# Optimization experiments

Hardware: AMD Instinct MI355X
Metric: run time of the kernel (lower is better)

Reference implementation:

```python
import jax, jax.numpy as jnp
import numpy as np

B, S, D, H, FF = 4, 2048, 512, 8, 2048
HD = D // H
WINDOW = 64  # local attention half-window in rank space
EPS = 1e-5


def _layer_norm(v, g, b):
    m = jnp.mean(v, axis=-1, keepdims=True)
    var = jnp.mean(jnp.square(v - m), axis=-1, keepdims=True)
    return (v - m) / jnp.sqrt(var + EPS) * g + b


def setup_inputs() -> dict:
    key = jax.random.key(0)
    ks = jax.random.split(key, 10)
    sc = 0.02
    x = jax.random.normal(ks[0], (B, S, D), jnp.float32)
    padding_mask = jnp.zeros((B, S), dtype=bool)
    i = jnp.arange(S)
    local = jnp.abs(i[:, None] - i[None, :]) <= WINDOW
    glob = (i[:, None] == 0) | (i[None, :] == 0)  # global spectrum token at pos 0
    attn_mask = jnp.where(local | glob, 0.0, -jnp.inf).astype(jnp.float32)
    return {
        "x": x,
        "padding_mask": padding_mask,
        "attn_mask": attn_mask,
        "in_proj_w": jax.random.normal(ks[1], (3 * D, D), jnp.float32) * sc,
        "in_proj_b": jnp.zeros((3 * D,), jnp.float32),
        "out_proj_w": jax.random.normal(ks[2], (D, D), jnp.float32) * sc,
        "out_proj_b": jnp.zeros((D,), jnp.float32),
        "ln1_g": jnp.ones((D,), jnp.float32),
        "ln1_b": jnp.zeros((D,), jnp.float32),
        "ln2_g": jnp.ones((D,), jnp.float32),
        "ln2_b": jnp.zeros((D,), jnp.float32),
        "ff_w1": jax.random.normal(ks[3], (FF, D), jnp.float32) * sc,
        "ff_b1": jnp.zeros((FF,), jnp.float32),
        "ff_w2": jax.random.normal(ks[4], (D, FF), jnp.float32) * sc,
        "ff_b2": jnp.zeros((D,), jnp.float32),
    }


def reference(x, padding_mask, attn_mask, in_proj_w, in_proj_b, out_proj_w,
              out_proj_b, ln1_g, ln1_b, ln2_g, ln2_b, ff_w1, ff_b1, ff_w2, ff_b2):
    # pre-LN attention
    a = _layer_norm(x, ln1_g, ln1_b)
    qkv = a @ in_proj_w.T + in_proj_b  # [B,S,3D]
    q, k, v = jnp.split(qkv, 3, axis=-1)
    to_heads = lambda t: t.reshape(B, S, H, HD).transpose(0, 2, 1, 3)
    q, k, v = to_heads(q), to_heads(k), to_heads(v)
    scores = jnp.einsum('bhqd,bhkd->bhqk', q, k) * (HD ** -0.5)
    # float attn_mask path: key_padding_mask converted to additive -inf floats
    kpm = jnp.where(padding_mask, -jnp.inf, 0.0).astype(scores.dtype)
    scores = scores + attn_mask[None, None, :, :] + kpm[:, None, None, :]
    p = jax.nn.softmax(scores, axis=-1)
    o = jnp.einsum('bhqk,bhkd->bhqd', p, v).transpose(0, 2, 1, 3).reshape(B, S, D)
    o = o @ out_proj_w.T + out_proj_b
    x = x + o  # residual (dropout = 0)
    # pre-LN feed-forward with exact GELU (torch nn.GELU default)
    f = _layer_norm(x, ln2_g, ln2_b)
    f = jax.nn.gelu(f @ ff_w1.T + ff_b1, approximate=False) @ ff_w2.T + ff_b2
    return x + f
```

## Files before the change

kernel.cpp:

```cpp
#include <hip/hip_runtime.h>
#include <hip/hip_bf16.h>
#include <math.h>

namespace {

constexpr int kB = 4, kS = 2048, kD = 512, kH = 8, kFF = 2048;
constexpr int kM = kB * kS;
constexpr int kHD = kD / kH;
constexpr int kWin = 64;

typedef __attribute__((ext_vector_type(8))) short short8;
typedef __attribute__((ext_vector_type(4))) float f32x4;

__device__ __forceinline__ float bf2f(__hip_bfloat16 v) { return __bfloat162float(v); }
__device__ __forceinline__ __hip_bfloat16 f2bf(float v) { return __float2bfloat16(v); }
__device__ __forceinline__ int iclamp(int v, int lo, int hi) { return v < lo ? lo : (v > hi ? hi : v); }

__device__ __forceinline__ void async16(const void* g, void* l) {
  __builtin_amdgcn_global_load_lds((const __attribute__((address_space(1))) void*)g,
                                   (__attribute__((address_space(3))) void*)l, 16, 0, 0);
}

__global__ __launch_bounds__(256)
void prep(const float* __restrict__ iw, const float* __restrict__ ow,
          const float* __restrict__ f1, const float* __restrict__ f2,
          __hip_bfloat16* __restrict__ wq, __hip_bfloat16* __restrict__ wo,
          __hip_bfloat16* __restrict__ w1, __hip_bfloat16* __restrict__ w2,
          const float* __restrict__ x, const float* __restrict__ g,
          const float* __restrict__ bta, __hip_bfloat16* __restrict__ a,
          __hip_bfloat16* __restrict__ xb) {
  const int id = blockIdx.x;
  if (id < 3072) {
    const float* s; __hip_bfloat16* d; int base;
    if (id < 768)       { s = iw; d = wq; base = id; }
    else if (id < 1024) { s = ow; d = wo; base = id - 768; }
    else if (id < 2048) { s = f1; d = w1; base = id - 1024; }
    else                { s = f2; d = w2; base = id - 2048; }
    int i = base * 1024 + threadIdx.x * 4;
    float4 v = *(const float4*)(s + i);
    union { __hip_bfloat16 h[4]; uint2 u; } t;
    t.h[0] = f2bf(v.x); t.h[1] = f2bf(v.y); t.h[2] = f2bf(v.z); t.h[3] = f2bf(v.w);
    *(uint2*)(d + i) = t.u;
  } else {
    int row = (id - 3072) * 4 + (threadIdx.x >> 6);
    int lane = threadIdx.x & 63;
    const float* xr = x + (size_t)row * kD;
    int c = lane * 8;
    float4 v0 = *(const float4*)(xr + c);
    float4 v1 = *(const float4*)(xr + c + 4);
    union { __hip_bfloat16 h[8]; int4 u; } xr8;
    xr8.h[0] = f2bf(v0.x); xr8.h[1] = f2bf(v0.y); xr8.h[2] = f2bf(v0.z); xr8.h[3] = f2bf(v0.w);
    xr8.h[4] = f2bf(v1.x); xr8.h[5] = f2bf(v1.y); xr8.h[6] = f2bf(v1.z); xr8.h[7] = f2bf(v1.w);
    *(int4*)(xb + (size_t)row * kD + c) = xr8.u;
    float s  = v0.x + v0.y + v0.z + v0.w + v1.x + v1.y + v1.z + v1.w;
    float ss = v0.x*v0.x + v0.y*v0.y + v0.z*v0.z + v0.w*v0.w
             + v1.x*v1.x + v1.y*v1.y + v1.z*v1.z + v1.w*v1.w;
#pragma unroll
    for (int o = 32; o > 0; o >>= 1) { s += __shfl_xor(s, o); ss += __shfl_xor(ss, o); }
    float mean = s * (1.0f / kD);
    float inv  = rsqrtf(ss * (1.0f / kD) - mean * mean + 1e-5f);
    float4 g0 = *(const float4*)(g + c),   g1 = *(const float4*)(g + c + 4);
    float4 b0 = *(const float4*)(bta + c), b1 = *(const float4*)(bta + c + 4);
    union { __hip_bfloat16 h[8]; int4 u; } t;
    t.h[0] = f2bf((v0.x - mean) * inv * g0.x + b0.x);
    t.h[1] = f2bf((v0.y - mean) * inv * g0.y + b0.y);
    t.h[2] = f2bf((v0.z - mean) * inv * g0.z + b0.z);
    t.h[3] = f2bf((v0.w - mean) * inv * g0.w + b0.w);
    t.h[4] = f2bf((v1.x - mean) * inv * g1.x + b1.x);
    t.h[5] = f2bf((v1.y - mean) * inv * g1.y + b1.y);
    t.h[6] = f2bf((v1.z - mean) * inv * g1.z + b1.z);
    t.h[7] = f2bf((v1.w - mean) * inv * g1.w + b1.w);
    *(int4*)(a + (size_t)row * kD + c) = t.u;
  }
}

__global__ __launch_bounds__(256)
void ln_rows_bf(const __hip_bfloat16* __restrict__ x, const float* __restrict__ g,
                const float* __restrict__ bta, __hip_bfloat16* __restrict__ out) {
  int row = blockIdx.x * 4 + (threadIdx.x >> 6);
  int lane = threadIdx.x & 63;
  int c = lane * 8;
  union { short8 v; __hip_bfloat16 hh[8]; } u;
  u.v = *(const short8*)(x + (size_t)row * kD + c);
  float f[8];
  float s = 0.f, ss = 0.f;
#pragma unroll
  for (int i = 0; i < 8; ++i) { f[i] = bf2f(u.hh[i]); s += f[i]; ss += f[i] * f[i]; }
#pragma unroll
  for (int o = 32; o > 0; o >>= 1) { s += __shfl_xor(s, o); ss += __shfl_xor(ss, o); }
  float mean = s * (1.0f / kD);
  float inv  = rsqrtf(ss * (1.0f / kD) - mean * mean + 1e-5f);
  float4 g0 = *(const float4*)(g + c),   g1 = *(const float4*)(g + c + 4);
  float4 b0 = *(const float4*)(bta + c), b1 = *(const float4*)(bta + c + 4);
  union { __hip_bfloat16 h[8]; int4 v; } t;
  t.h[0] = f2bf((f[0] - mean) * inv * g0.x + b0.x);
  t.h[1] = f2bf((f[1] - mean) * inv * g0.y + b0.y);
  t.h[2] = f2bf((f[2] - mean) * inv * g0.z + b0.z);
  t.h[3] = f2bf((f[3] - mean) * inv * g0.w + b0.w);
  t.h[4] = f2bf((f[4] - mean) * inv * g1.x + b1.x);
  t.h[5] = f2bf((f[5] - mean) * inv * g1.y + b1.y);
  t.h[6] = f2bf((f[6] - mean) * inv * g1.z + b1.z);
  t.h[7] = f2bf((f[7] - mean) * inv * g1.w + b1.w);
  *(int4*)(out + (size_t)row * kD + c) = t.v;
}

__global__ __launch_bounds__(256)
void attn_tile(const __hip_bfloat16* __restrict__ qkv, const __hip_bfloat16* __restrict__ vt,
               __hip_bfloat16* __restrict__ o) {
  const int bh = blockIdx.x;
  const int b = bh >> 3, h = bh & 7;
  const int tid = threadIdx.x;
  const int lane = tid & 63, w = tid >> 6;

  __shared__ alignas(16) char smem[4 * 160 * 20 * 2];

  const __hip_bfloat16* base = qkv + (size_t)b * kS * (3 * kD);
  const __hip_bfloat16* vt_bh = vt + (size_t)(b * kH + h) * kHD * kS;

  if (blockIdx.y == 0) {
    float* sc   = (float*)smem;
    float* qs   = sc + 2048;
    float* redm = qs + 64;
    float* reds = redm + 4;
    float* part = reds + 4;
    if (tid < kHD) qs[tid] = bf2f(base[h * kHD + tid]) * 0.125f;
    __syncthreads();

    float m = -1e30f;
#pragma unroll
    for (int it = 0; it < 8; ++it) {
      int k = it * 256 + tid;
      const short8* kp = (const short8*)(base + (size_t)k * (3 * kD) + kD + h * kHD);
      float s = 0.f;
#pragma unroll
      for (int cc = 0; cc < 8; ++cc) {
        union { short8 v; __hip_bfloat16 hh[8]; } u;
        u.v = kp[cc];
#pragma unroll
        for (int d = 0; d < 8; ++d) s += qs[cc * 8 + d] * bf2f(u.hh[d]);
      }
      sc[k] = s;
      m = fmaxf(m, s);
    }
#pragma unroll
    for (int off = 32; off > 0; off >>= 1) m = fmaxf(m, __shfl_xor(m, off));
    if (lane == 0) redm[w] = m;
    __syncthreads();
    float M = fmaxf(fmaxf(redm[0], redm[1]), fmaxf(redm[2], redm[3]));

    float ls = 0.f;
#pragma unroll
    for (int it = 0; it < 8; ++it) {
      int k = it * 256 + tid;
      float e = __expf(sc[k] - M);
      sc[k] = e;
      ls += e;
    }
#pragma unroll
    for (int off = 32; off > 0; off >>= 1) ls += __shfl_xor(ls, off);
    if (lane == 0) reds[w] = ls;
    __syncthreads();
    float L = reds[0] + reds[1] + reds[2] + reds[3];

    float a0 = 0.f, a1 = 0.f;
    const __hip_bfloat16* vr = vt_bh + (size_t)lane * kS + w * 512;
#pragma unroll
    for (int c = 0; c < 64; c += 2) {
      union { short8 v; __hip_bfloat16 hh[8]; } u0, u1;
      u0.v = *(const short8*)(vr + c * 8);
      u1.v = *(const short8*)(vr + c * 8 + 8);
#pragma unroll
      for (int j = 0; j < 8; ++j) {
        a0 += sc[w * 512 + c * 8 + j] * bf2f(u0.hh[j]);
        a1 += sc[w * 512 + c * 8 + 8 + j] * bf2f(u1.hh[j]);
      }
    }
    part[w * 64 + lane] = a0 + a1;
    __syncthreads();
    if (tid < kHD) {
      float s = part[tid] + part[64 + tid] + part[128 + tid] + part[192 + tid];
      o[(size_t)(b * kS) * kD + h * kHD + tid] = f2bf(s / L);
    }
    return;
  }

  const int tq = (blockIdx.y - 1) * 4 + w;
  const int quad = lane >> 4, col = lane & 15;
  const int q0 = tq * 16;
  const int kbase = q0 - kWin;
  __hip_bfloat16* Pt = (__hip_bfloat16*)smem + w * 160 * 20;

  short8 aq0, aq1;
  {
    const __hip_bfloat16* qrow = base + (size_t)(q0 + col) * (3 * kD) + h * kHD + quad * 8;
    aq0 = *(const short8*)qrow;
    aq1 = *(const short8*)(qrow + 32);
  }

  f32x4 sc[10];
#pragma unroll
  for (int t = 0; t < 10; ++t) {
    int krow = (t < 9) ? iclamp(kbase + t * 16 + col, 0, kS - 1) : col;
    const short8* kp = (const short8*)(base + (size_t)krow * (3 * kD) + kD + h * kHD + quad * 8);
    f32x4 a = (f32x4){0.f, 0.f, 0.f, 0.f};
    a = __builtin_amdgcn_mfma_f32_16x16x32_bf16(aq0, kp[0], a, 0, 0, 0);
    a = __builtin_amdgcn_mfma_f32_16x16x32_bf16(aq1, kp[4], a, 0, 0, 0);
    sc[t] = a;
  }

  float rowmax[4] = {-1e30f, -1e30f, -1e30f, -1e30f};
#pragma unroll
  for (int t = 0; t < 10; ++t) {
#pragma unroll
    for (int r = 0; r < 4; ++r) {
      int q = q0 + quad * 4 + r;
      bool valid;
      if (t < 9) {
        int k = kbase + t * 16 + col;
        valid = (k >= 0) && (k < kS) && ((q - k <= kWin && k - q <= kWin) || k == 0);
      } else {
        valid = (col == 0) && (kbase > 0);
      }
      float s = valid ? sc[t][r] * 0.125f : -1e30f;
      sc[t][r] = s;
      rowmax[r] = fmaxf(rowmax[r], s);
    }
  }
#pragma unroll
  for (int r = 0; r < 4; ++r)
#pragma unroll
    for (int off = 1; off < 16; off <<= 1)
      rowmax[r] = fmaxf(rowmax[r], __shfl_xor(rowmax[r], off));

  float rowsum[4] = {0.f, 0.f, 0.f, 0.f};
#pragma unroll
  for (int t = 0; t < 10; ++t)
#pragma unroll
    for (int r = 0; r < 4; ++r) {
      float e = __expf(sc[t][r] - rowmax[r]);
      sc[t][r] = e;
      rowsum[r] += e;
    }
#pragma unroll
  for (int r = 0; r < 4; ++r)
#pragma unroll
    for (int off = 1; off < 16; off <<= 1)
      rowsum[r] += __shfl_xor(rowsum[r], off);

#pragma unroll
  for (int t = 0; t < 10; ++t) {
    union { ushort u[4]; unsigned long long ll; } pk;
#pragma unroll
    for (int r = 0; r < 4; ++r) {
      __hip_bfloat16 hv = f2bf(sc[t][r]);
      pk.u[r] = *(ushort*)&hv;
    }
    *(unsigned long long*)&Pt[(t * 16 + col) * 20 + quad * 4] = pk.ll;
  }

  f32x4 oacc[4];
#pragma unroll
  for (int n = 0; n < 4; ++n) oacc[n] = (f32x4){0.f, 0.f, 0.f, 0.f};

#pragma unroll
  for (int c = 0; c < 5; ++c) {
    union { short s[8]; short8 v; } pa;
#pragma unroll
    for (int j = 0; j < 8; ++j) pa.s[j] = *(const short*)&Pt[(c * 32 + quad * 8 + j) * 20 + col];
    const int kc = c * 32 + quad * 8;
    const int kstart = (kc < 144) ? iclamp(kbase + kc, 0, kS - 8) : (kc - 144);
#pragma unroll
    for (int n = 0; n < 4; ++n) {
      short8 vb = *(const short8*)(vt_bh + (size_t)(n * 16 + col) * kS + kstart);
      oacc[n] = __builtin_amdgcn_mfma_f32_16x16x32_bf16(pa.v, vb, oacc[n], 0, 0, 0);
    }
  }

#pragma unroll
  for (int n = 0; n < 4; ++n)
#pragma unroll
    for (int r = 0; r < 4; ++r) {
      int q = q0 + quad * 4 + r;
      if (q == 0) continue;
      o[(size_t)(b * kS + q) * kD + h * kHD + n * 16 + col] = f2bf(oacc[n][r] / rowsum[r]);
    }
}

template <int TM, int TN, int NB, int EPI, int WVT, typename OT, typename RT>
__global__ __launch_bounds__(256, 4)
void gemm_bt(const __hip_bfloat16* __restrict__ A, const __hip_bfloat16* __restrict__ W,
             const float* __restrict__ bias, const RT* __restrict__ resid,
             OT* __restrict__ C, __hip_bfloat16* __restrict__ vt, int Ndim, int K) {
  constexpr int MI = TM / 32;
  constexpr int NF = TN / 32;
  __shared__ __hip_bfloat16 As[TM * 64];
  __shared__ __hip_bfloat16 Ws[TN * 64];

  const int id = blockIdx.x;
  const int rr = id & 7, tt = id >> 3;
  const int nb = tt % NB, mb = (tt / NB) * 8 + rr;

  const int tid = threadIdx.x;
  const int lane = tid & 63, w = tid >> 6;
  const int wm = w >> 1, wn = w & 1;
  const int quad = lane >> 4, mrow = lane & 15;
  const int m0 = mb * TM, n0 = nb * TN;

  const int lrow = lane >> 3;
  const int lcol = ((lane & 7) ^ lrow) << 3;

  f32x4 acc[MI][NF];
#pragma unroll
  for (int i = 0; i < MI; ++i)
#pragma unroll
    for (int j = 0; j < NF; ++j) acc[i][j] = (f32x4){0.f, 0.f, 0.f, 0.f};

  for (int kt = 0; kt < K; kt += 64) {
#pragma unroll
    for (int it = 0; it < MI; ++it) {
      int c = w * MI + it;
      async16(A + (size_t)(m0 + c * 8 + lrow) * K + kt + lcol, &As[c * 512]);
    }
#pragma unroll
    for (int it = 0; it < NF; ++it) {
      int c = w * NF + it;
      async16(W + (size_t)(n0 + c * 8 + lrow) * K + kt + lcol, &Ws[c * 512]);
    }
    __syncthreads();
#pragma unroll
    for (int kk = 0; kk < 64; kk += 32) {
      const int ch = (kk >> 3) + quad;
      const int sw = (ch ^ (mrow & 7)) << 3;
      short8 af[MI], wf[NF];
#pragma unroll
      for (int i = 0; i < MI; ++i)
        af[i] = *(const short8*)&As[(wm * (TM / 2) + i * 16 + mrow) * 64 + sw];
#pragma unroll
      for (int j = 0; j < NF; ++j)
        wf[j] = *(const short8*)&Ws[(wn * (TN / 2) + j * 16 + mrow) * 64 + sw];
#pragma unroll
      for (int i = 0; i < MI; ++i)
#pragma unroll
        for (int j = 0; j < NF; ++j)
          acc[i][j] = __builtin_amdgcn_mfma_f32_16x16x32_bf16(af[i], wf[j], acc[i][j], 0, 0, 0);
    }
    __syncthreads();
  }

  if constexpr (WVT) {
    if (n0 >= 1024) {
      __hip_bfloat16* Ls = As;
      const int bb = m0 >> 11, ss0 = m0 & (kS - 1);
      const int n0v = n0 - 1024;
#pragma unroll
      for (int p = 0; p < 2; ++p) {
        __syncthreads();
#pragma unroll
        for (int jj = 0; jj < 2; ++jj) {
          int j = p * 2 + jj;
          int lr = wn * 32 + jj * 16 + mrow;
          float bs = bias[1024 + n0v + wn * 64 + j * 16 + mrow];
#pragma unroll
          for (int i = 0; i < 4; ++i) {
            int tok = wm * 64 + i * 16 + quad * 4;
            int tw = tok ^ ((lr & 15) << 3);
            union { __hip_bfloat16 h[4]; unsigned long long u; } pk;
#pragma unroll
            for (int r = 0; r < 4; ++r) pk.h[r] = f2bf(acc[i][j][r] + bs);
            *(unsigned long long*)&Ls[lr * 128 + tw] = pk.u;
          }
        }
        __syncthreads();
#pragma unroll
        for (int i2 = 0; i2 < 4; ++i2) {
          int c = i2 * 256 + tid;
          int lr = c >> 4, off = (c & 15) << 3;
          int tw = off ^ ((lr & 15) << 3);
          short8 v = *(const short8*)&Ls[lr * 128 + tw];
          int colv = (lr >> 5) * 64 + p * 32 + (lr & 31);
          *(short8*)(vt + (size_t)(bb * 512 + n0v + colv) * kS + ss0 + off) = v;
        }
      }
      return;
    }
  }

#pragma unroll
  for (int i = 0; i < MI; ++i) {
#pragma unroll
    for (int r = 0; r < 4; ++r) {
      int row = m0 + wm * (TM / 2) + i * 16 + quad * 4 + r;
#pragma unroll
      for (int j = 0; j < NF; ++j) {
        int col = n0 + wn * (TN / 2) + j * 16 + mrow;
        float v = acc[i][j][r] + bias[col];
        if (EPI == 1) v = 0.5f * v * (1.0f + erff(v * 0.70710678118f));
        if (EPI == 3) v += bf2f(((const __hip_bfloat16*)resid)[(size_t)row * Ndim + col]);
        if constexpr (__is_same(OT, float)) C[(size_t)row * Ndim + col] = v;
        else                                C[(size_t)row * Ndim + col] = f2bf(v);
      }
    }
  }
}

}

extern "C" void kernel_launch(void* const* d_in, const int* in_sizes, int n_in,
                              void* d_out, int out_size, void* d_ws, size_t ws_size,
                              hipStream_t stream) {
  const float* x          = (const float*)d_in[0];
  const float* in_proj_w  = (const float*)d_in[3];
  const float* in_proj_b  = (const float*)d_in[4];
  const float* out_proj_w = (const float*)d_in[5];
  const float* out_proj_b = (const float*)d_in[6];
  const float* ln1_g      = (const float*)d_in[7];
  const float* ln1_b      = (const float*)d_in[8];
  const float* ln2_g      = (const float*)d_in[9];
  const float* ln2_b      = (const float*)d_in[10];
  const float* ff_w1      = (const float*)d_in[11];
  const float* ff_b1      = (const float*)d_in[12];
  const float* ff_w2      = (const float*)d_in[13];
  const float* ff_b2      = (const float*)d_in[14];
  float* out = (float*)d_out;

  char* ws = (char*)d_ws;
  size_t off = 0;
  auto carve = [&](size_t bytes) { char* p = ws + off; off += (bytes + 255) & ~(size_t)255; return p; };
  __hip_bfloat16* wqkv_bf = (__hip_bfloat16*)carve((size_t)3 * kD * kD * 2);
  __hip_bfloat16* wout_bf = (__hip_bfloat16*)carve((size_t)kD * kD * 2);
  __hip_bfloat16* wff1_bf = (__hip_bfloat16*)carve((size_t)kFF * kD * 2);
  __hip_bfloat16* wff2_bf = (__hip_bfloat16*)carve((size_t)kD * kFF * 2);
  __hip_bfloat16* a_bf    = (__hip_bfloat16*)carve((size_t)kM * kD * 2);
  __hip_bfloat16* x_bf    = (__hip_bfloat16*)carve((size_t)kM * kD * 2);
  __hip_bfloat16* qkv_bf  = (__hip_bfloat16*)carve((size_t)kM * 3 * kD * 2);
  __hip_bfloat16* vt      = (__hip_bfloat16*)carve((size_t)kM * kD * 2);
  __hip_bfloat16* o_bf    = (__hip_bfloat16*)carve((size_t)kM * kD * 2);
  __hip_bfloat16* r1b     = (__hip_bfloat16*)carve((size_t)kM * kD * 2);
  __hip_bfloat16* ln2_bf  = (__hip_bfloat16*)carve((size_t)kM * kD * 2);
  __hip_bfloat16* ff1_bf  = (__hip_bfloat16*)carve((size_t)kM * kFF * 2);

  prep<<<5120, 256, 0, stream>>>(in_proj_w, out_proj_w, ff_w1, ff_w2,
                                 wqkv_bf, wout_bf, wff1_bf, wff2_bf,
                                 x, ln1_g, ln1_b, a_bf, x_bf);
  gemm_bt<128, 128, 12, 0, 1, __hip_bfloat16, float><<<64 * 12, 256, 0, stream>>>(
      a_bf, wqkv_bf, in_proj_b, nullptr, qkv_bf, vt, 3 * kD, kD);
  attn_tile<<<dim3(kB * kH, kS / 64 + 1), 256, 0, stream>>>(qkv_bf, vt, o_bf);
  gemm_bt<64, 64, 8, 3, 0, __hip_bfloat16, __hip_bfloat16><<<128 * 8, 256, 0, stream>>>(
      o_bf, wout_bf, out_proj_b, x_bf, r1b, nullptr, kD, kD);
  ln_rows_bf<<<kM / 4, 256, 0, stream>>>(r1b, ln2_g, ln2_b, ln2_bf);
  gemm_bt<128, 128, 16, 1, 0, __hip_bfloat16, float><<<64 * 16, 256, 0, stream>>>(
      ln2_bf, wff1_bf, ff_b1, nullptr, ff1_bf, nullptr, kFF, kD);
  gemm_bt<64, 64, 8, 3, 0, float, __hip_bfloat16><<<128 * 8, 256, 0, stream>>>(
      ff1_bf, wff2_bf, ff_b2, r1b, out, nullptr, kD, kFF);
}
```

Measured before the change: 239.1 us.

## Stage shared K tile in LDS for local attention and restructure global-row dot

```diff
diff --git a/kernel.cpp b/kernel.cpp
--- a/kernel.cpp
+++ b/kernel.cpp
@@ -112,34 +112,36 @@
   const int tid = threadIdx.x;
   const int lane = tid & 63, w = tid >> 6;
 
-  __shared__ alignas(16) char smem[4 * 160 * 20 * 2];
+  __shared__ alignas(16) char smem[26880];
 
   const __hip_bfloat16* base = qkv + (size_t)b * kS * (3 * kD);
   const __hip_bfloat16* vt_bh = vt + (size_t)(b * kH + h) * kHD * kS;
 
   if (blockIdx.y == 0) {
     float* sc   = (float*)smem;
-    float* qs   = sc + 2048;
-    float* redm = qs + 64;
+    float* redm = sc + 2048;
     float* reds = redm + 4;
     float* part = reds + 4;
-    if (tid < kHD) qs[tid] = bf2f(base[h * kHD + tid]) * 0.125f;
-    __syncthreads();
-
+    const int j8 = lane >> 3, p8 = lane & 7;
+
+    float qf[8];
+    {
+      union { short8 v; __hip_bfloat16 hh[8]; } uq;
+      uq.v = *(const short8*)(base + h * kHD + p8 * 8);
+#pragma unroll
+      for (int d = 0; d < 8; ++d) qf[d] = bf2f(uq.hh[d]) * 0.125f;
+    }
     float m = -1e30f;
-#pragma unroll
-    for (int it = 0; it < 8; ++it) {
-      int k = it * 256 + tid;
-      const short8* kp = (const short8*)(base + (size_t)k * (3 * kD) + kD + h * kHD);
+#pragma unroll 4
+    for (int it = 0; it < 64; ++it) {
+      int k = w * 512 + it * 8 + j8;
+      union { short8 v; __hip_bfloat16 hh[8]; } uk;
+      uk.v = *(const short8*)(base + (size_t)k * (3 * kD) + kD + h * kHD + p8 * 8);
       float s = 0.f;
 #pragma unroll
-      for (int cc = 0; cc < 8; ++cc) {
-        union { short8 v; __hip_bfloat16 hh[8]; } u;
-        u.v = kp[cc];
-#pragma unroll
-        for (int d = 0; d < 8; ++d) s += qs[cc * 8 + d] * bf2f(u.hh[d]);
-      }
-      sc[k] = s;
+      for (int d = 0; d < 8; ++d) s += qf[d] * bf2f(uk.hh[d]);
+      s += __shfl_xor(s, 1); s += __shfl_xor(s, 2); s += __shfl_xor(s, 4);
+      if (p8 == 0) sc[k] = s;
       m = fmaxf(m, s);
     }
 #pragma unroll
@@ -162,20 +164,18 @@
     __syncthreads();
     float L = reds[0] + reds[1] + reds[2] + reds[3];
 
-    float a0 = 0.f, a1 = 0.f;
+    float a = 0.f;
     const __hip_bfloat16* vr = vt_bh + (size_t)lane * kS + w * 512;
-#pragma unroll
-    for (int c = 0; c < 64; c += 2) {
-      union { short8 v; __hip_bfloat16 hh[8]; } u0, u1;
-      u0.v = *(const short8*)(vr + c * 8);
-      u1.v = *(const short8*)(vr + c * 8 + 8);
-#pragma unroll
-      for (int j = 0; j < 8; ++j) {
-        a0 += sc[w * 512 + c * 8 + j] * bf2f(u0.hh[j]);
-        a1 += sc[w * 512 + c * 8 + 8 + j] * bf2f(u1.hh[j]);
-      }
-    }
-    part[w * 64 + lane] = a0 + a1;
+#pragma unroll 8
+    for (int c = 0; c < 64; ++c) {
+      union { short8 v; __hip_bfloat16 hh[8]; } u;
+      u.v = *(const short8*)(vr + c * 8);
+      float4 s0 = *(const float4*)&sc[w * 512 + c * 8];
+      float4 s1 = *(const float4*)&sc[w * 512 + c * 8 + 4];
+      a += s0.x * bf2f(u.hh[0]) + s0.y * bf2f(u.hh[1]) + s0.z * bf2f(u.hh[2]) + s0.w * bf2f(u.hh[3])
+         + s1.x * bf2f(u.hh[4]) + s1.y * bf2f(u.hh[5]) + s1.z * bf2f(u.hh[6]) + s1.w * bf2f(u.hh[7]);
+    }
+    part[w * 64 + lane] = a;
     __syncthreads();
     if (tid < kHD) {
       float s = part[tid] + part[64 + tid] + part[128 + tid] + part[192 + tid];
@@ -184,11 +184,28 @@
     return;
   }
 
-  const int tq = (blockIdx.y - 1) * 4 + w;
+  const int g = blockIdx.y - 1;
+  const int kbase0 = g * 64 - kWin;
   const int quad = lane >> 4, col = lane & 15;
+  const int tq = g * 4 + w;
   const int q0 = tq * 16;
-  const int kbase = q0 - kWin;
-  __hip_bfloat16* Pt = (__hip_bfloat16*)smem + w * 160 * 20;
+  const int kbw = q0 - kWin;
+
+  __hip_bfloat16* Ks = (__hip_bfloat16*)smem;
+  __hip_bfloat16* Pt = (__hip_bfloat16*)smem + w * 3200;
+
+  {
+    const int lrow8 = lane >> 3;
+    const int scol = (((lane & 7) ^ lrow8) << 3);
+#pragma unroll
+    for (int i = 0; i < 7; ++i) {
+      int c = w + 4 * i;
+      if (c < 26) {
+        int key = (c < 24) ? iclamp(kbase0 + c * 8 + lrow8, 0, kS - 1) : ((c - 24) * 8 + lrow8);
+        async16(base + (size_t)key * (3 * kD) + kD + h * kHD + scol, &Ks[c * 512]);
+      }
+    }
+  }
 
   short8 aq0, aq1;
   {
@@ -196,15 +213,17 @@
     aq0 = *(const short8*)qrow;
     aq1 = *(const short8*)(qrow + 32);
   }
+  __syncthreads();
 
   f32x4 sc[10];
 #pragma unroll
   for (int t = 0; t < 10; ++t) {
-    int krow = (t < 9) ? iclamp(kbase + t * 16 + col, 0, kS - 1) : col;
-    const short8* kp = (const short8*)(base + (size_t)krow * (3 * kD) + kD + h * kHD + quad * 8);
+    int rel = (t < 9) ? (w * 16 + t * 16 + col) : (192 + col);
+    short8 k0 = *(const short8*)&Ks[rel * 64 + ((quad ^ (rel & 7)) << 3)];
+    short8 k1 = *(const short8*)&Ks[rel * 64 + (((quad + 4) ^ (rel & 7)) << 3)];
     f32x4 a = (f32x4){0.f, 0.f, 0.f, 0.f};
-    a = __builtin_amdgcn_mfma_f32_16x16x32_bf16(aq0, kp[0], a, 0, 0, 0);
-    a = __builtin_amdgcn_mfma_f32_16x16x32_bf16(aq1, kp[4], a, 0, 0, 0);
+    a = __builtin_amdgcn_mfma_f32_16x16x32_bf16(aq0, k0, a, 0, 0, 0);
+    a = __builtin_amdgcn_mfma_f32_16x16x32_bf16(aq1, k1, a, 0, 0, 0);
     sc[t] = a;
   }
 
@@ -216,10 +235,10 @@
       int q = q0 + quad * 4 + r;
       bool valid;
       if (t < 9) {
-        int k = kbase + t * 16 + col;
+        int k = kbw + t * 16 + col;
         valid = (k >= 0) && (k < kS) && ((q - k <= kWin && k - q <= kWin) || k == 0);
       } else {
-        valid = (col == 0) && (kbase > 0);
+        valid = (col == 0) && (kbw > 0);
       }
       float s = valid ? sc[t][r] * 0.125f : -1e30f;
       sc[t][r] = s;
@@ -247,6 +266,8 @@
     for (int off = 1; off < 16; off <<= 1)
       rowsum[r] += __shfl_xor(rowsum[r], off);
 
+  __syncthreads();
+
 #pragma unroll
   for (int t = 0; t < 10; ++t) {
     union { ushort u[4]; unsigned long long ll; } pk;
@@ -268,7 +289,7 @@
 #pragma unroll
     for (int j = 0; j < 8; ++j) pa.s[j] = *(const short*)&Pt[(c * 32 + quad * 8 + j) * 20 + col];
     const int kc = c * 32 + quad * 8;
-    const int kstart = (kc < 144) ? iclamp(kbase + kc, 0, kS - 8) : (kc - 144);
+    const int kstart = (kc < 144) ? iclamp(kbw + kc, 0, kS - 8) : (kc - 144);
 #pragma unroll
     for (int n = 0; n < 4; ++n) {
       short8 vb = *(const short8*)(vt_bh + (size_t)(n * 16 + col) * kS + kstart);
```

Measured after the change: 237.0 us. About the same (-0.9%).
